# Kernel tuning notes

Hardware: AMD Instinct MI355X
Metric: run time of the kernel (lower is better)

Reference implementation:

```python
import jax, jax.numpy as jnp
import numpy as np

EMBED = 1024
HEADS = 16
HEAD_DIM = EMBED // HEADS


def setup_inputs() -> dict:
    key = jax.random.key(0)
    ks = jax.random.split(key, 9)
    s = 0.02
    return {
        "hidden_states": jax.random.normal(ks[0], (1, 4, 1500, EMBED), dtype=jnp.float32),
        "q_w": jax.random.normal(ks[1], (EMBED, EMBED), dtype=jnp.float32) * s,
        "q_b": jax.random.normal(ks[2], (EMBED,), dtype=jnp.float32) * s,
        "k_w": jax.random.normal(ks[3], (EMBED, EMBED), dtype=jnp.float32) * s,
        "v_w": jax.random.normal(ks[4], (EMBED, EMBED), dtype=jnp.float32) * s,
        "v_b": jax.random.normal(ks[5], (EMBED,), dtype=jnp.float32) * s,
        "out_w": jax.random.normal(ks[6], (EMBED, EMBED), dtype=jnp.float32) * s,
        "out_b": jax.random.normal(ks[7], (EMBED,), dtype=jnp.float32) * s,
    }


def reference(hidden_states, q_w, q_b, k_w, v_w, v_b, out_w, out_b):
    # hidden_states: [1, B, S, E]
    _, bsz, tgt_len, _ = hidden_states.shape
    x = hidden_states[0]  # [B, S, E]
    scaling = HEAD_DIM ** -0.5

    def split_heads(t):  # [B, S, E] -> [B, H, S, Dh]
        return t.reshape(bsz, tgt_len, HEADS, HEAD_DIM).transpose(0, 2, 1, 3)

    # Linear layers use torch convention: y = x @ W.T + b  (k_proj has no bias)
    q = split_heads((x @ q_w.T + q_b) * scaling)
    k = split_heads(x @ k_w.T)
    v = split_heads(x @ v_w.T + v_b)

    # attention scores [B, H, S, S]
    attn_weights = jnp.einsum("bhqd,bhkd->bhqk", q, k)
    attn_probs = jax.nn.softmax(attn_weights, axis=-1)
    attn_out = jnp.einsum("bhqk,bhkd->bhqd", attn_probs, v)  # [B, H, S, Dh]

    attn_out = attn_out.transpose(0, 2, 1, 3).reshape(1, bsz, tgt_len, EMBED)
    return attn_out @ out_w.T + out_b
```

## Files before the change

kernel.cpp:

```cpp
#include <hip/hip_runtime.h>
#include <cstddef>
#include <cstdint>

#define EMB 1024
#define SEQ 1500
#define NB 4
#define NH 16
#define DH 64
#define MTOT (NB*SEQ)
#define VTS 1536

typedef __bf16 bf16;
typedef __bf16 bf16x4 __attribute__((ext_vector_type(4)));
typedef __bf16 bf16x8 __attribute__((ext_vector_type(8)));
typedef short  s16x4  __attribute__((ext_vector_type(4)));
typedef float  f32x4  __attribute__((ext_vector_type(4)));

#define LOG2E 1.44269504088896340736f

__device__ __forceinline__ void async16(const void* g, const void* l) {
    __builtin_amdgcn_global_load_lds(
        (const __attribute__((address_space(1))) uint32_t*)g,
        (__attribute__((address_space(3))) uint32_t*)l, 16, 0, 0);
}

__device__ __forceinline__ uint32_t pack_bf16_trunc(float e0, float e1) {
    return __builtin_amdgcn_perm(__builtin_bit_cast(uint32_t, e1),
                                 __builtin_bit_cast(uint32_t, e0), 0x07060302u);
}

struct CvtArgs {
    const float* xs; bf16* xd;
    const float* w[4]; bf16* wd[4];
};

__global__ __launch_bounds__(256) void cvt_kernel(CvtArgs a) {
    const size_t NX = (size_t)MTOT * EMB;
    const size_t NW = (size_t)EMB * EMB;
    const size_t tot = NX + 4 * NW;
    for (size_t i = ((size_t)blockIdx.x * 256 + threadIdx.x) * 4; i < tot;
         i += (size_t)gridDim.x * 1024) {
        const float* s; bf16* d; size_t off;
        if (i < NX) { s = a.xs; d = a.xd; off = i; }
        else {
            size_t j = i - NX;
            int wi = (int)(j >> 20);
            off = j & (NW - 1);
            s = a.w[wi]; d = a.wd[wi];
        }
        float4 v = *(const float4*)(s + off);
        bf16x4 o = { (bf16)v.x, (bf16)v.y, (bf16)v.z, (bf16)v.w };
        *(bf16x4*)(d + off) = o;
    }
}

__global__ __launch_bounds__(256) void gemm_fused(
    const bf16* __restrict__ X,
    const bf16* __restrict__ W0, const bf16* __restrict__ W1, const bf16* __restrict__ W2,
    const float* __restrict__ b_q, const float* __restrict__ b_v,
    bf16* __restrict__ Oq, bf16* __restrict__ Ok, bf16* __restrict__ Ovt,
    int M)
{
    __shared__ bf16 As[2][128 * 32];
    __shared__ bf16 Bs[2][128 * 32];
    const int tid = threadIdx.x;
    const int lane = tid & 63, w = tid >> 6;
    const int q = lane >> 4, lr = lane & 15;
    const int wr = w >> 1, wc = w & 1;

    const int id = blockIdx.x;
    const int t_ = id >> 3;
    const int mtile = (id & 7) + (t_ % 6) * 8;
    const int y = t_ / 6;
    const int m0 = mtile * 128;
    const int proj = y >> 3;
    const int n0 = (y & 7) * 128;

    const bf16 *PA, *PB;
    int baseA, baseB, limA, limB;
    if (proj == 2) {
        PA = X;  baseA = m0; limA = M;
        PB = W2; baseB = n0; limB = EMB;
    } else {
        PA = (proj == 0) ? W0 : W1;
        baseA = n0; limA = EMB;
        PB = X; baseB = m0; limB = M;
    }

    f32x4 acc[4][4] = {};

    const int srow = w * 32 + (lane >> 2);
    const int swz_ch = (((lane & 3) ^ ((lane >> 3) & 3))) * 8;
    const bf16* pA[2]; const bf16* pB[2];
#pragma unroll
    for (int i = 0; i < 2; i++) {
        int ra = baseA + srow + i * 16; ra = ra < limA ? ra : limA - 1;
        int rb = baseB + srow + i * 16; rb = rb < limB ? rb : limB - 1;
        pA[i] = PA + (size_t)ra * EMB + swz_ch;
        pB[i] = PB + (size_t)rb * EMB + swz_ch;
    }

#pragma unroll
    for (int i = 0; i < 2; i++) {
        async16(pA[i], As[0] + (w * 2 + i) * 512);
        async16(pB[i], Bs[0] + (w * 2 + i) * 512);
    }

    const int qsw = (q ^ ((lr >> 1) & 3)) * 8;
    const int arow = (wr * 64 + lr) * 32;
    const int brow = (wc * 64 + lr) * 32;

    for (int k0 = 0; k0 < EMB; k0 += 32) {
        const int cur = (k0 >> 5) & 1;
        __syncthreads();
        const int nxt = k0 + 32;
        if (nxt < EMB) {
#pragma unroll
            for (int i = 0; i < 2; i++) {
                async16(pA[i] + nxt, As[cur ^ 1] + (w * 2 + i) * 512);
                async16(pB[i] + nxt, Bs[cur ^ 1] + (w * 2 + i) * 512);
            }
        }
        const bf16* Ab = As[cur];
        const bf16* Bb = Bs[cur];
        bf16x8 af[4], bfr[4];
#pragma unroll
        for (int t = 0; t < 4; t++) {
            af[t]  = *(const bf16x8*)(Ab + arow + t * 512 + qsw);
            bfr[t] = *(const bf16x8*)(Bb + brow + t * 512 + qsw);
        }
#pragma unroll
        for (int ti = 0; ti < 4; ti++)
#pragma unroll
            for (int tj = 0; tj < 4; tj++)
                acc[ti][tj] = __builtin_amdgcn_mfma_f32_16x16x32_bf16(
                    af[ti], bfr[tj], acc[ti][tj], 0, 0, 0);
    }

    if (proj <= 1) {
        const float scale = (proj == 0) ? 0.125f * LOG2E : 1.0f;
        const float* bias = (proj == 0) ? b_q : nullptr;
        bf16* O = (proj == 0) ? Oq : Ok;
#pragma unroll
        for (int tj = 0; tj < 4; tj++) {
            const int m = m0 + wc * 64 + tj * 16 + lr;
            if (m >= M) continue;
            const int b_ = m / SEQ, s_ = m % SEQ;
#pragma unroll
            for (int ti = 0; ti < 4; ti++) {
                const int nb = n0 + wr * 64 + ti * 16 + q * 4;
                const int h = nb >> 6, d = nb & 63;
                float4 b4 = bias ? *(const float4*)(bias + nb)
                                 : make_float4(0.f, 0.f, 0.f, 0.f);
                bf16x4 o;
                o[0] = (bf16)((acc[ti][tj][0] + b4.x) * scale);
                o[1] = (bf16)((acc[ti][tj][1] + b4.y) * scale);
                o[2] = (bf16)((acc[ti][tj][2] + b4.z) * scale);
                o[3] = (bf16)((acc[ti][tj][3] + b4.w) * scale);
                *(bf16x4*)(O + (((size_t)b_ * NH + h) * SEQ + s_) * DH + d) = o;
            }
        }
    } else {
#pragma unroll
        for (int ti = 0; ti < 4; ti++) {
            const int mb = m0 + wr * 64 + ti * 16 + q * 4;
            if (mb >= M) continue;
            const int b_ = mb / SEQ, s_ = mb % SEQ;
#pragma unroll
            for (int tj = 0; tj < 4; tj++) {
                const int nb = n0 + wc * 64 + tj * 16 + lr;
                const int h = nb >> 6, d = nb & 63;
                const float bv = b_v[nb];
                bf16x4 o;
                o[0] = (bf16)(acc[ti][tj][0] + bv);
                o[1] = (bf16)(acc[ti][tj][1] + bv);
                o[2] = (bf16)(acc[ti][tj][2] + bv);
                o[3] = (bf16)(acc[ti][tj][3] + bv);
                *(bf16x4*)(Ovt + ((size_t)(b_ * NH + h) * DH + d) * VTS + s_) = o;
            }
        }
    }
}

__global__ __launch_bounds__(256) void gemm_out(
    const bf16* __restrict__ X, const bf16* __restrict__ Wo,
    const float* __restrict__ b_o, float* __restrict__ Of, int M)
{
    __shared__ bf16 As[2][64 * 32];
    __shared__ bf16 Bs[2][128 * 32];
    const int tid = threadIdx.x;
    const int lane = tid & 63, w = tid >> 6;
    const int q = lane >> 4, lr = lane & 15;
    const int wc = w & 1, wr = w >> 1;

    const int id = blockIdx.x;
    const int xcd = id & 7;
    const int h = id >> 3;
    const int mtile = (h % 6) * 8 + xcd;
    const int ntile = h / 6;
    const int m0 = mtile * 128, n0 = ntile * 64;

    const int cs = ((tid & 3) ^ ((tid >> 3) & 3)) * 8;
    const bf16* pA = Wo + (size_t)(n0 + (tid >> 2)) * EMB + cs;
    const int srow = w * 32 + (lane >> 2);
    const bf16* pB[2];
#pragma unroll
    for (int i = 0; i < 2; i++) {
        int rb = m0 + srow + i * 16; rb = rb < M ? rb : M - 1;
        pB[i] = X + (size_t)rb * EMB + cs;
    }

    async16(pA, As[0] + w * 512);
#pragma unroll
    for (int i = 0; i < 2; i++)
        async16(pB[i], Bs[0] + (w * 2 + i) * 512);

    f32x4 acc[2][4] = {};
    const int qsw = (q ^ ((lr >> 1) & 3)) * 8;
    const int arow = (wr * 32 + lr) * 32;
    const int brow = (wc * 64 + lr) * 32;

    for (int k0 = 0; k0 < EMB; k0 += 32) {
        const int cur = (k0 >> 5) & 1;
        __syncthreads();
        const int nxt = k0 + 32;
        if (nxt < EMB) {
            async16(pA + nxt, As[cur ^ 1] + w * 512);
#pragma unroll
            for (int i = 0; i < 2; i++)
                async16(pB[i] + nxt, Bs[cur ^ 1] + (w * 2 + i) * 512);
        }
        bf16x8 af[2], bfr[4];
#pragma unroll
        for (int t = 0; t < 2; t++)
            af[t] = *(const bf16x8*)(As[cur] + arow + t * 512 + qsw);
#pragma unroll
        for (int t = 0; t < 4; t++)
            bfr[t] = *(const bf16x8*)(Bs[cur] + brow + t * 512 + qsw);
#pragma unroll
        for (int ti = 0; ti < 2; ti++)
#pragma unroll
            for (int tj = 0; tj < 4; tj++)
                acc[ti][tj] = __builtin_amdgcn_mfma_f32_16x16x32_bf16(
                    af[ti], bfr[tj], acc[ti][tj], 0, 0, 0);
    }

#pragma unroll
    for (int tj = 0; tj < 4; tj++) {
        const int m = m0 + wc * 64 + tj * 16 + lr;
        if (m >= M) continue;
#pragma unroll
        for (int ti = 0; ti < 2; ti++) {
            const int nb = n0 + wr * 32 + ti * 16 + q * 4;
            const float4 b4 = *(const float4*)(b_o + nb);
            float4 o;
            o.x = acc[ti][tj][0] + b4.x;
            o.y = acc[ti][tj][1] + b4.y;
            o.z = acc[ti][tj][2] + b4.z;
            o.w = acc[ti][tj][3] + b4.w;
            *(float4*)(Of + (size_t)m * EMB + nb) = o;
        }
    }
}

__global__ __launch_bounds__(256) void attn_mfma(
    const bf16* __restrict__ Qb, const bf16* __restrict__ Kb,
    const bf16* __restrict__ Vt, bf16* __restrict__ ctx)
{
    __shared__ bf16 Ks[2][64 * 64];
    __shared__ bf16 Vs[2][64 * 64];
    const int tid = threadIdx.x;
    const int lane = tid & 63, w = tid >> 6;
    const int q = lane >> 4, lr = lane & 15;
    const int bh = blockIdx.x, b_ = bh >> 4, h_ = bh & 15;
    const int q0 = blockIdx.y * 128;
    const size_t base = (size_t)bh * SEQ * DH;
    const size_t vbase = (size_t)bh * DH * VTS;

    int qrow[2];
    bf16x8 qf[2][2];
#pragma unroll
    for (int g = 0; g < 2; g++) {
        qrow[g] = q0 + g * 64 + w * 16 + lr;
        const int qrc = qrow[g] < SEQ ? qrow[g] : (SEQ - 1);
        qf[g][0] = *(const bf16x8*)(Qb + base + (size_t)qrc * DH + q * 8);
        qf[g][1] = *(const bf16x8*)(Qb + base + (size_t)qrc * DH + 32 + q * 8);
    }

    f32x4 oacc[2][4] = {};
    f32x4 lacc[2] = {};
    const s16x4 ones = { (short)0x3F80, (short)0x3F80, (short)0x3F80, (short)0x3F80 };

    const int srow = tid >> 3;
    const int sch8 = ((tid & 7) ^ (srow & 7)) * 8;
    const int kswz = lr & 7;

    const int NT = (SEQ + 63) / 64;

    {
        int r0 = srow, r1 = srow + 32;
        async16(Kb + base + (size_t)r0 * DH + sch8, Ks[0] + tid * 8);
        async16(Kb + base + (size_t)r1 * DH + sch8, Ks[0] + tid * 8 + 2048);
        async16(Vt + vbase + (size_t)srow * VTS + sch8,        Vs[0] + tid * 8);
        async16(Vt + vbase + (size_t)(srow + 32) * VTS + sch8, Vs[0] + tid * 8 + 2048);
    }

    for (int kt = 0; kt < NT; kt++) {
        const int k0 = kt * 64;
        const int cur = kt & 1;
        __syncthreads();

        if (kt + 1 < NT) {
            const int kn = k0 + 64;
            int r0 = kn + srow;      if (r0 >= SEQ) r0 = SEQ - 1;
            int r1 = kn + srow + 32; if (r1 >= SEQ) r1 = SEQ - 1;
            async16(Kb + base + (size_t)r0 * DH + sch8, Ks[cur ^ 1] + tid * 8);
            async16(Kb + base + (size_t)r1 * DH + sch8, Ks[cur ^ 1] + tid * 8 + 2048);
            async16(Vt + vbase + (size_t)srow * VTS + kn + sch8,
                    Vs[cur ^ 1] + tid * 8);
            async16(Vt + vbase + (size_t)(srow + 32) * VTS + kn + sch8,
                    Vs[cur ^ 1] + tid * 8 + 2048);
        }

        const bf16* Kc = Ks[cur];
        const bf16* Vc = Vs[cur];

        bf16x8 kf[2][4];
#pragma unroll
        for (int s = 0; s < 2; s++)
#pragma unroll
            for (int mt = 0; mt < 4; mt++)
                kf[s][mt] = *(const bf16x8*)(Kc + (mt * 16 + lr) * 64 +
                                             ((4 * s + q) ^ kswz) * 8);

        s16x4 pf[2][4];
#pragma unroll
        for (int g = 0; g < 2; g++) {
            f32x4 st[4] = {};
#pragma unroll
            for (int s = 0; s < 2; s++)
#pragma unroll
                for (int mt = 0; mt < 4; mt++)
                    st[mt] = __builtin_amdgcn_mfma_f32_16x16x32_bf16(
                        kf[s][mt], qf[g][s], st[mt], 0, 0, 0);

            if (k0 + 64 > SEQ) {
#pragma unroll
                for (int mt = 0; mt < 4; mt++)
#pragma unroll
                    for (int r = 0; r < 4; r++)
                        if (k0 + mt * 16 + q * 4 + r >= SEQ) st[mt][r] = -16384.0f;
            }

#pragma unroll
            for (int mt = 0; mt < 4; mt++) {
                float e0 = __builtin_amdgcn_exp2f(st[mt][0]);
                float e1 = __builtin_amdgcn_exp2f(st[mt][1]);
                float e2 = __builtin_amdgcn_exp2f(st[mt][2]);
                float e3 = __builtin_amdgcn_exp2f(st[mt][3]);
                uint32_t lo = pack_bf16_trunc(e0, e1);
                uint32_t hi = pack_bf16_trunc(e2, e3);
                uint2 pk = { lo, hi };
                pf[g][mt] = __builtin_bit_cast(s16x4, pk);
            }
#pragma unroll
            for (int c = 0; c < 4; c++)
                lacc[g] = __builtin_amdgcn_mfma_f32_16x16x16bf16_1k(
                    ones, pf[g][c], lacc[g], 0, 0, 0);
        }

#pragma unroll
        for (int c = 0; c < 4; c++) {
#pragma unroll
            for (int dt = 0; dt < 4; dt++) {
                const s16x4 vf = __builtin_bit_cast(s16x4,
                    *(const bf16x4*)(Vc + (dt * 16 + lr) * 64 +
                                     ((2 * c + (q >> 1)) ^ kswz) * 8 + (q & 1) * 4));
                oacc[0][dt] = __builtin_amdgcn_mfma_f32_16x16x16bf16_1k(
                    vf, pf[0][c], oacc[0][dt], 0, 0, 0);
                oacc[1][dt] = __builtin_amdgcn_mfma_f32_16x16x16bf16_1k(
                    vf, pf[1][c], oacc[1][dt], 0, 0, 0);
            }
        }
    }

#pragma unroll
    for (int g = 0; g < 2; g++) {
        const float inv = 1.0f / lacc[g][0];
        if (qrow[g] < SEQ) {
            const size_t rowoff = ((size_t)b_ * SEQ + qrow[g]) * EMB + h_ * DH;
#pragma unroll
            for (int dt = 0; dt < 4; dt++) {
                bf16x4 o;
#pragma unroll
                for (int r = 0; r < 4; r++) o[r] = (bf16)(oacc[g][dt][r] * inv);
                *(bf16x4*)(ctx + rowoff + dt * 16 + q * 4) = o;
            }
        }
    }
}

extern "C" void kernel_launch(void* const* d_in, const int* in_sizes, int n_in,
                              void* d_out, int out_size, void* d_ws, size_t ws_size,
                              hipStream_t stream) {
    const float* x     = (const float*)d_in[0];
    const float* q_w   = (const float*)d_in[1];
    const float* q_b   = (const float*)d_in[2];
    const float* k_w   = (const float*)d_in[3];
    const float* v_w   = (const float*)d_in[4];
    const float* v_b   = (const float*)d_in[5];
    const float* out_w = (const float*)d_in[6];
    const float* out_b = (const float*)d_in[7];
    float* out = (float*)d_out;

    const size_t nbuf = (size_t)MTOT * EMB;
    const size_t nvt  = (size_t)NB * NH * DH * VTS;
    const size_t nw   = (size_t)EMB * EMB;
    bf16* xb  = (bf16*)d_ws;
    bf16* qws = xb  + nbuf;
    bf16* kws = qws + nbuf;
    bf16* vtw = kws + nbuf;
    bf16* wqb = vtw + nvt;
    bf16* wkb = wqb + nw;
    bf16* wvb = wkb + nw;
    bf16* wob = wvb + nw;
    bf16* ctx = xb;

    CvtArgs ca;
    ca.xs = x;      ca.xd = xb;
    ca.w[0] = q_w;  ca.wd[0] = wqb;
    ca.w[1] = k_w;  ca.wd[1] = wkb;
    ca.w[2] = v_w;  ca.wd[2] = wvb;
    ca.w[3] = out_w; ca.wd[3] = wob;
    cvt_kernel<<<dim3(2560), 256, 0, stream>>>(ca);

    gemm_fused<<<dim3(48 * 24), 256, 0, stream>>>(
        xb, wqb, wkb, wvb, q_b, v_b, qws, kws, vtw, MTOT);

    attn_mfma<<<dim3(NB * NH, (SEQ + 127) / 128), 256, 0, stream>>>(qws, kws, vtw, ctx);

    gemm_out<<<dim3(768), 256, 0, stream>>>(ctx, wob, out_b, out, MTOT);
}
```

Baseline: 241.3 us.

## Use two-wave blocks with larger per-wave tiles in projection GEMMs

Both GEMM kernels drop from four waves per block to two. Each wave now computes a larger sub-tile: 128x64 in the fused QKV GEMM and 64x64 in the output GEMM. This raises register-level reuse of LDS fragments and halves the number of waves contending on each block barrier. The cost is higher accumulator register pressure (32 MFMA accumulators per wave in gemm_fused) and fewer waves per block to hide load latency.

```diff
diff --git a/kernel.cpp b/kernel.cpp
--- a/kernel.cpp
+++ b/kernel.cpp
@@ -54,7 +54,7 @@
     }
 }
 
-__global__ __launch_bounds__(256) void gemm_fused(
+__global__ __launch_bounds__(128) void gemm_fused(
     const bf16* __restrict__ X,
     const bf16* __restrict__ W0, const bf16* __restrict__ W1, const bf16* __restrict__ W2,
     const float* __restrict__ b_q, const float* __restrict__ b_v,
@@ -66,7 +66,6 @@
     const int tid = threadIdx.x;
     const int lane = tid & 63, w = tid >> 6;
     const int q = lane >> 4, lr = lane & 15;
-    const int wr = w >> 1, wc = w & 1;
 
     const int id = blockIdx.x;
     const int t_ = id >> 3;
@@ -87,28 +86,25 @@
         PB = X; baseB = m0; limB = M;
     }
 
-    f32x4 acc[4][4] = {};
-
-    const int srow = w * 32 + (lane >> 2);
-    const int swz_ch = (((lane & 3) ^ ((lane >> 3) & 3))) * 8;
-    const bf16* pA[2]; const bf16* pB[2];
-#pragma unroll
-    for (int i = 0; i < 2; i++) {
-        int ra = baseA + srow + i * 16; ra = ra < limA ? ra : limA - 1;
-        int rb = baseB + srow + i * 16; rb = rb < limB ? rb : limB - 1;
-        pA[i] = PA + (size_t)ra * EMB + swz_ch;
-        pB[i] = PB + (size_t)rb * EMB + swz_ch;
-    }
-
-#pragma unroll
-    for (int i = 0; i < 2; i++) {
-        async16(pA[i], As[0] + (w * 2 + i) * 512);
-        async16(pB[i], Bs[0] + (w * 2 + i) * 512);
+    f32x4 acc[8][4] = {};
+
+    const int swz_ch = ((lane & 3) ^ ((lane >> 3) & 3)) * 8;
+    const bf16* pA[4]; const bf16* pB[4];
+#pragma unroll
+    for (int j = 0; j < 4; j++) {
+        int ra = baseA + (w * 4 + j) * 16 + (lane >> 2); ra = ra < limA ? ra : limA - 1;
+        int rb = baseB + (w * 4 + j) * 16 + (lane >> 2); rb = rb < limB ? rb : limB - 1;
+        pA[j] = PA + (size_t)ra * EMB + swz_ch;
+        pB[j] = PB + (size_t)rb * EMB + swz_ch;
+    }
+
+#pragma unroll
+    for (int j = 0; j < 4; j++) {
+        async16(pA[j], As[0] + (w * 4 + j) * 512);
+        async16(pB[j], Bs[0] + (w * 4 + j) * 512);
     }
 
     const int qsw = (q ^ ((lr >> 1) & 3)) * 8;
-    const int arow = (wr * 64 + lr) * 32;
-    const int brow = (wc * 64 + lr) * 32;
 
     for (int k0 = 0; k0 < EMB; k0 += 32) {
         const int cur = (k0 >> 5) & 1;
@@ -116,21 +112,22 @@
         const int nxt = k0 + 32;
         if (nxt < EMB) {
 #pragma unroll
-            for (int i = 0; i < 2; i++) {
-                async16(pA[i] + nxt, As[cur ^ 1] + (w * 2 + i) * 512);
-                async16(pB[i] + nxt, Bs[cur ^ 1] + (w * 2 + i) * 512);
+            for (int j = 0; j < 4; j++) {
+                async16(pA[j] + nxt, As[cur ^ 1] + (w * 4 + j) * 512);
+                async16(pB[j] + nxt, Bs[cur ^ 1] + (w * 4 + j) * 512);
             }
         }
         const bf16* Ab = As[cur];
         const bf16* Bb = Bs[cur];
-        bf16x8 af[4], bfr[4];
-#pragma unroll
-        for (int t = 0; t < 4; t++) {
-            af[t]  = *(const bf16x8*)(Ab + arow + t * 512 + qsw);
-            bfr[t] = *(const bf16x8*)(Bb + brow + t * 512 + qsw);
-        }
-#pragma unroll
-        for (int ti = 0; ti < 4; ti++)
+        bf16x8 af[8], bfr[4];
+#pragma unroll
+        for (int t = 0; t < 8; t++)
+            af[t] = *(const bf16x8*)(Ab + (t * 16 + lr) * 32 + qsw);
+#pragma unroll
+        for (int t = 0; t < 4; t++)
+            bfr[t] = *(const bf16x8*)(Bb + (w * 64 + t * 16 + lr) * 32 + qsw);
+#pragma unroll
+        for (int ti = 0; ti < 8; ti++)
 #pragma unroll
             for (int tj = 0; tj < 4; tj++)
                 acc[ti][tj] = __builtin_amdgcn_mfma_f32_16x16x32_bf16(
@@ -143,12 +140,12 @@
         bf16* O = (proj == 0) ? Oq : Ok;
 #pragma unroll
         for (int tj = 0; tj < 4; tj++) {
-            const int m = m0 + wc * 64 + tj * 16 + lr;
+            const int m = m0 + w * 64 + tj * 16 + lr;
             if (m >= M) continue;
             const int b_ = m / SEQ, s_ = m % SEQ;
 #pragma unroll
-            for (int ti = 0; ti < 4; ti++) {
-                const int nb = n0 + wr * 64 + ti * 16 + q * 4;
+            for (int ti = 0; ti < 8; ti++) {
+                const int nb = n0 + ti * 16 + q * 4;
                 const int h = nb >> 6, d = nb & 63;
                 float4 b4 = bias ? *(const float4*)(bias + nb)
                                  : make_float4(0.f, 0.f, 0.f, 0.f);
@@ -162,13 +159,13 @@
         }
     } else {
 #pragma unroll
-        for (int ti = 0; ti < 4; ti++) {
-            const int mb = m0 + wr * 64 + ti * 16 + q * 4;
+        for (int ti = 0; ti < 8; ti++) {
+            const int mb = m0 + ti * 16 + q * 4;
             if (mb >= M) continue;
             const int b_ = mb / SEQ, s_ = mb % SEQ;
 #pragma unroll
             for (int tj = 0; tj < 4; tj++) {
-                const int nb = n0 + wc * 64 + tj * 16 + lr;
+                const int nb = n0 + w * 64 + tj * 16 + lr;
                 const int h = nb >> 6, d = nb & 63;
                 const float bv = b_v[nb];
                 bf16x4 o;
@@ -182,7 +179,7 @@
     }
 }
 
-__global__ __launch_bounds__(256) void gemm_out(
+__global__ __launch_bounds__(128) void gemm_out(
     const bf16* __restrict__ X, const bf16* __restrict__ Wo,
     const float* __restrict__ b_o, float* __restrict__ Of, int M)
 {
@@ -191,7 +188,6 @@
     const int tid = threadIdx.x;
     const int lane = tid & 63, w = tid >> 6;
     const int q = lane >> 4, lr = lane & 15;
-    const int wc = w & 1, wr = w >> 1;
 
     const int id = blockIdx.x;
     const int xcd = id & 7;
@@ -200,45 +196,48 @@
     const int ntile = h / 6;
     const int m0 = mtile * 128, n0 = ntile * 64;
 
-    const int cs = ((tid & 3) ^ ((tid >> 3) & 3)) * 8;
-    const bf16* pA = Wo + (size_t)(n0 + (tid >> 2)) * EMB + cs;
-    const int srow = w * 32 + (lane >> 2);
-    const bf16* pB[2];
-#pragma unroll
-    for (int i = 0; i < 2; i++) {
-        int rb = m0 + srow + i * 16; rb = rb < M ? rb : M - 1;
-        pB[i] = X + (size_t)rb * EMB + cs;
-    }
-
-    async16(pA, As[0] + w * 512);
-#pragma unroll
-    for (int i = 0; i < 2; i++)
-        async16(pB[i], Bs[0] + (w * 2 + i) * 512);
-
-    f32x4 acc[2][4] = {};
+    const int swz_ch = ((lane & 3) ^ ((lane >> 3) & 3)) * 8;
+    const bf16* pA[2]; const bf16* pB[4];
+#pragma unroll
+    for (int j = 0; j < 2; j++) {
+        int ra = n0 + (w * 2 + j) * 16 + (lane >> 2);
+        pA[j] = Wo + (size_t)ra * EMB + swz_ch;
+    }
+#pragma unroll
+    for (int j = 0; j < 4; j++) {
+        int rb = m0 + (w * 4 + j) * 16 + (lane >> 2); rb = rb < M ? rb : M - 1;
+        pB[j] = X + (size_t)rb * EMB + swz_ch;
+    }
+
+#pragma unroll
+    for (int j = 0; j < 2; j++) async16(pA[j], As[0] + (w * 2 + j) * 512);
+#pragma unroll
+    for (int j = 0; j < 4; j++) async16(pB[j], Bs[0] + (w * 4 + j) * 512);
+
+    f32x4 acc[4][4] = {};
     const int qsw = (q ^ ((lr >> 1) & 3)) * 8;
-    const int arow = (wr * 32 + lr) * 32;
-    const int brow = (wc * 64 + lr) * 32;
 
     for (int k0 = 0; k0 < EMB; k0 += 32) {
         const int cur = (k0 >> 5) & 1;
         __syncthreads();
         const int nxt = k0 + 32;
         if (nxt < EMB) {
-            async16(pA + nxt, As[cur ^ 1] + w * 512);
-#pragma unroll
-            for (int i = 0; i < 2; i++)
-                async16(pB[i] + nxt, Bs[cur ^ 1] + (w * 2 + i) * 512);
-        }
-        bf16x8 af[2], bfr[4];
-#pragma unroll
-        for (int t = 0; t < 2; t++)
-            af[t] = *(const bf16x8*)(As[cur] + arow + t * 512 + qsw);
+#pragma unroll
+            for (int j = 0; j < 2; j++)
+                async16(pA[j] + nxt, As[cur ^ 1] + (w * 2 + j) * 512);
+#pragma unroll
+            for (int j = 0; j < 4; j++)
+                async16(pB[j] + nxt, Bs[cur ^ 1] + (w * 4 + j) * 512);
+        }
+        bf16x8 af[4], bfr[4];
 #pragma unroll
         for (int t = 0; t < 4; t++)
-            bfr[t] = *(const bf16x8*)(Bs[cur] + brow + t * 512 + qsw);
-#pragma unroll
-        for (int ti = 0; ti < 2; ti++)
+            af[t] = *(const bf16x8*)(As[cur] + (t * 16 + lr) * 32 + qsw);
+#pragma unroll
+        for (int t = 0; t < 4; t++)
+            bfr[t] = *(const bf16x8*)(Bs[cur] + (w * 64 + t * 16 + lr) * 32 + qsw);
+#pragma unroll
+        for (int ti = 0; ti < 4; ti++)
 #pragma unroll
             for (int tj = 0; tj < 4; tj++)
                 acc[ti][tj] = __builtin_amdgcn_mfma_f32_16x16x32_bf16(
@@ -247,11 +246,11 @@
 
 #pragma unroll
     for (int tj = 0; tj < 4; tj++) {
-        const int m = m0 + wc * 64 + tj * 16 + lr;
+        const int m = m0 + w * 64 + tj * 16 + lr;
         if (m >= M) continue;
 #pragma unroll
-        for (int ti = 0; ti < 2; ti++) {
-            const int nb = n0 + wr * 32 + ti * 16 + q * 4;
+        for (int ti = 0; ti < 4; ti++) {
+            const int nb = n0 + ti * 16 + q * 4;
             const float4 b4 = *(const float4*)(b_o + nb);
             float4 o;
             o.x = acc[ti][tj][0] + b4.x;
@@ -434,10 +433,10 @@
     ca.w[3] = out_w; ca.wd[3] = wob;
     cvt_kernel<<<dim3(2560), 256, 0, stream>>>(ca);
 
-    gemm_fused<<<dim3(48 * 24), 256, 0, stream>>>(
+    gemm_fused<<<dim3(48 * 24), 128, 0, stream>>>(
         xb, wqb, wkb, wvb, q_b, v_b, qws, kws, vtw, MTOT);
 
     attn_mfma<<<dim3(NB * NH, (SEQ + 127) / 128), 256, 0, stream>>>(qws, kws, vtw, ctx);
 
-    gemm_out<<<dim3(768), 256, 0, stream>>>(ctx, wob, out_b, out, MTOT);
-}
+    gemm_out<<<dim3(768), 128, 0, stream>>>(ctx, wob, out_b, out, MTOT);
+}
```

Result: slower. 265.5 us (+10.1%).
